# Kernel tuning notes

Measured on AMD Instinct MI355X. Metric: run time of the kernel, lower is better.

The kernel has to match this reference:

```python
import jax, jax.numpy as jnp
import numpy as np

B1, B2, D = 8192, 8192, 128


def _cdist(d1, d2):
    # L2 distance matrix via the |a|^2 + |b|^2 - 2ab expansion (GEMM-dominant).
    d1_sq = jnp.sum(d1 * d1, axis=1, keepdims=True)          # (B1, 1)
    d2_sq = jnp.sum(d2 * d2, axis=1, keepdims=True)          # (B2, 1)
    dm = d1_sq + d2_sq.T - 2.0 * (d1 @ d2.T)                 # (B1, B2)
    return jnp.sqrt(jnp.clip(dm, 0.0))


def setup_inputs() -> dict:
    key = jax.random.key(0)
    k1, k2 = jax.random.split(key)
    desc1 = jax.random.normal(k1, (B1, D), dtype=jnp.float32)
    desc2 = jax.random.normal(k2, (B2, D), dtype=jnp.float32)
    return {"desc1": desc1, "desc2": desc2}


def reference(desc1, desc2):
    # DescriptorMatcher(match_mode='nn'): nearest neighbor in desc2 for each desc1.
    dm = _cdist(desc1, desc2)                                # (B1, B2)
    idxs_in_2 = jnp.argmin(dm, axis=1)                       # (B1,)
    match_dists = jnp.take_along_axis(dm, idxs_in_2[:, None], axis=1)  # (B1, 1)
    idxs_in_1 = jnp.arange(dm.shape[0], dtype=jnp.int64 if jax.config.jax_enable_x64 else jnp.int32)
    matches_idxs = jnp.stack([idxs_in_1, idxs_in_2.astype(idxs_in_1.dtype)], axis=1)  # (B1, 2)
    return match_dists, matches_idxs
```

## Files before the change

kernel.cpp:

```cpp
#include <hip/hip_runtime.h>
#include <cstdint>

#define NB1 8192
#define NB2 8192
#define DDIM 128
#define KROW 256
#define NKITER 12

using half8   = __attribute__((ext_vector_type(8))) _Float16;
using half4   = __attribute__((ext_vector_type(4))) _Float16;
using float4v = __attribute__((ext_vector_type(4))) float;

typedef __attribute__((address_space(3))) void       lds_void;
typedef const __attribute__((address_space(1))) void glb_void;

__device__ inline unsigned long long packkey(float v, int j) {
  unsigned u = __float_as_uint(v);
  u = (u & 0x80000000u) ? ~u : (u | 0x80000000u);
  return ((unsigned long long)u << 32) | (unsigned)j;
}

__device__ __forceinline__ int a_src(int kt) { return (kt < 8) ? kt : kt - 8; }
__device__ __forceinline__ int b_src(int kt) { return (kt < 4) ? kt : kt - 4; }

__global__ __launch_bounds__(256) void convert_kernel(
    const float* __restrict__ d1, const float* __restrict__ d2,
    _Float16* __restrict__ A2, _Float16* __restrict__ B2,
    float* __restrict__ asq, float* __restrict__ bsq,
    unsigned long long* __restrict__ packed) {
  int gid  = blockIdx.x * 256 + threadIdx.x;
  int wv   = gid >> 6;
  int lane = gid & 63;
  int rowc = 2 * wv + (lane >> 5);
  bool isA = rowc < NB1;
  const float* src = isA ? d1 : d2;
  int row = isA ? rowc : rowc - NB1;
  int k4  = (lane & 31) * 4;

  float4 v = *(const float4*)&src[row * DDIM + k4];
  _Float16 h0 = (_Float16)v.x, h1 = (_Float16)v.y;
  _Float16 h2 = (_Float16)v.z, h3 = (_Float16)v.w;
  half4 hh = {h0, h1, h2, h3};
  half4 ll = {(_Float16)(v.x - (float)h0), (_Float16)(v.y - (float)h1),
              (_Float16)(v.z - (float)h2), (_Float16)(v.w - (float)h3)};

  _Float16* dst = (isA ? A2 : B2) + (size_t)row * KROW;
  *(half4*)&dst[k4]       = hh;
  *(half4*)&dst[128 + k4] = ll;

  float s = v.x * v.x + v.y * v.y + v.z * v.z + v.w * v.w;
  #pragma unroll
  for (int off = 16; off > 0; off >>= 1) s += __shfl_xor(s, off, 64);
  if ((lane & 31) == 0) (isA ? asq : bsq)[row] = s;

  if (gid < NB1) packed[gid] = 0xFFFFFFFFFFFFFFFFull;
}

__global__ __launch_bounds__(256, 3) void mfma_match_kernel(
    const _Float16* __restrict__ A2, const _Float16* __restrict__ B2,
    const float* __restrict__ bsq, unsigned long long* __restrict__ packed) {
  __shared__ unsigned long long smem[2 * 128 * 17];
  _Float16* Asb = (_Float16*)smem;
  _Float16* Bsb = (_Float16*)smem + 8192;

  const int t    = threadIdx.x;
  const int lane = t & 63;
  const int wid  = t >> 6;
  const int wm = wid >> 1, wn = wid & 1;
  const int lx = lane & 15, q = lane >> 4;

  const int id = blockIdx.x;
  const int xc = id & 7, kk = id >> 3;
  const int bx = ((kk >> 3) & 7) * 8 + xc;
  const int by = (kk & 7) + ((kk >> 6) & 7) * 8;
  const int row0 = bx * 128, col0 = by * 128;

  const int sA   = wid * 2;
  const int rloc = lane >> 2;
  const int qch  = ((lane & 3) - (rloc >> 1)) & 3;
  const int rA0  = sA * 16 + rloc;
  const int kofs = qch * 8;

  float4v acc[4][4];
  #pragma unroll
  for (int r = 0; r < 4; ++r)
    #pragma unroll
    for (int c = 0; c < 4; ++c) acc[r][c] = (float4v){0.f, 0.f, 0.f, 0.f};

  float bq[4]; int jc[4];
  #pragma unroll
  for (int c = 0; c < 4; ++c) {
    jc[c] = col0 + wn * 64 + 16 * c + lx;
    bq[c] = bsq[jc[c]];
  }

  auto stage = [&](int kt, int buf) {
    const _Float16* ga =
        A2 + (size_t)(row0 + rA0) * KROW + a_src(kt) * 32 + kofs;
    __builtin_amdgcn_global_load_lds((glb_void*)ga,
        (lds_void*)(Asb + buf * 4096 + sA * 512), 16, 0, 0);
    __builtin_amdgcn_global_load_lds((glb_void*)(ga + 16 * KROW),
        (lds_void*)(Asb + buf * 4096 + (sA + 1) * 512), 16, 0, 0);
    const _Float16* gb =
        B2 + (size_t)(col0 + rA0) * KROW + b_src(kt) * 32 + kofs;
    __builtin_amdgcn_global_load_lds((glb_void*)gb,
        (lds_void*)(Bsb + buf * 4096 + sA * 512), 16, 0, 0);
    __builtin_amdgcn_global_load_lds((glb_void*)(gb + 16 * KROW),
        (lds_void*)(Bsb + buf * 4096 + (sA + 1) * 512), 16, 0, 0);
  };

  stage(0, 0);

  const int sw = ((q + (lx >> 1)) & 3) * 8;

  #pragma unroll
  for (int kt = 0; kt < NKITER; ++kt) {
    __syncthreads();
    if (kt < NKITER - 1) stage(kt + 1, (kt + 1) & 1);
    const _Float16* Ab = Asb + (kt & 1) * 4096;
    const _Float16* Bb = Bsb + (kt & 1) * 4096;
    half8 af[4], bf[4];
    #pragma unroll
    for (int r = 0; r < 4; ++r)
      af[r] = *(const half8*)&Ab[(wm * 64 + 16 * r + lx) * 32 + sw];
    #pragma unroll
    for (int c = 0; c < 4; ++c)
      bf[c] = *(const half8*)&Bb[(wn * 64 + 16 * c + lx) * 32 + sw];
    #pragma unroll
    for (int r = 0; r < 4; ++r)
      #pragma unroll
      for (int c = 0; c < 4; ++c)
        acc[r][c] = __builtin_amdgcn_mfma_f32_16x16x32_f16(
            af[r], bf[c], acc[r][c], 0, 0, 0);
  }

  __syncthreads();
  #pragma unroll
  for (int r = 0; r < 4; ++r) {
    #pragma unroll
    for (int reg = 0; reg < 4; ++reg) {
      float bv = 1e30f; int bj = 0;
      #pragma unroll
      for (int c = 0; c < 4; ++c) {
        float val = fmaf(-2.f, acc[r][c][reg], bq[c]);
        if (val < bv) { bv = val; bj = jc[c]; }
      }
      int mrow = wm * 64 + 16 * r + 4 * q + reg;
      smem[(wn * 128 + mrow) * 17 + lx] = packkey(bv, bj);
    }
  }
  __syncthreads();
  if (t < 128) {
    unsigned long long best = ~0ull;
    #pragma unroll
    for (int w = 0; w < 2; ++w)
      #pragma unroll
      for (int x = 0; x < 16; ++x) {
        unsigned long long k = smem[(w * 128 + t) * 17 + x];
        if (k < best) best = k;
      }
    atomicMin(&packed[row0 + t], best);
  }
}

__global__ __launch_bounds__(256) void out_kernel(
    const unsigned long long* __restrict__ packed,
    const float* __restrict__ asq, float* __restrict__ out) {
  int r = blockIdx.x * 256 + threadIdx.x;
  unsigned long long best = packed[r];
  unsigned u = (unsigned)(best >> 32);
  u = (u & 0x80000000u) ? (u & 0x7fffffffu) : ~u;
  float val  = __uint_as_float(u);
  float dist = sqrtf(fmaxf(asq[r] + val, 0.f));
  int j = (int)(unsigned)(best & 0xffffffffu);
  out[r]               = dist;
  out[NB1 + 2 * r]     = (float)r;
  out[NB1 + 2 * r + 1] = (float)j;
}

extern "C" void kernel_launch(void* const* d_in, const int* in_sizes, int n_in,
                              void* d_out, int out_size, void* d_ws, size_t ws_size,
                              hipStream_t stream) {
  const float* d1 = (const float*)d_in[0];
  const float* d2 = (const float*)d_in[1];
  float* out = (float*)d_out;

  char* w = (char*)d_ws;
  float* asq = (float*)w;
  float* bsq = (float*)(w + 32768);
  _Float16* A2 = (_Float16*)(w + 65536);
  _Float16* B2 = (_Float16*)(w + 65536 + 4194304);
  unsigned long long* packed =
      (unsigned long long*)(w + 65536 + 2 * 4194304);

  convert_kernel<<<(NB1 + NB2) / 8, 256, 0, stream>>>(
      d1, d2, A2, B2, asq, bsq, packed);

  mfma_match_kernel<<<(NB1 / 128) * (NB2 / 128), 256, 0, stream>>>(
      A2, B2, bsq, packed);

  out_kernel<<<NB1 / 256, 256, 0, stream>>>(packed, asq, out);
}
```

Before: 123.5 us.

## Double K-tile depth per stage and fuse output finalization via last-block counter

Each main-loop stage now loads a 64-wide K slab instead of 32 and issues two MFMAs per fragment pair, which halves the number of barrier-separated iterations. LDS per block grows to 64KB and occupancy drops from 3 to 2 blocks per CU, with a wider XOR swizzle over 8 chunks. The separate output kernel is removed: a per-row-block atomic counter lets the last finishing column block decode the packed argmin and write distances and indices. This saves one launch but adds a fence and atomics at the end of every block.

```diff
diff --git a/kernel.cpp b/kernel.cpp
--- a/kernel.cpp
+++ b/kernel.cpp
@@ -5,7 +5,7 @@
 #define NB2 8192
 #define DDIM 128
 #define KROW 256
-#define NKITER 12
+#define NKITER 6
 
 using half8   = __attribute__((ext_vector_type(8))) _Float16;
 using half4   = __attribute__((ext_vector_type(4))) _Float16;
@@ -20,14 +20,14 @@
   return ((unsigned long long)u << 32) | (unsigned)j;
 }
 
-__device__ __forceinline__ int a_src(int kt) { return (kt < 8) ? kt : kt - 8; }
-__device__ __forceinline__ int b_src(int kt) { return (kt < 4) ? kt : kt - 4; }
+__device__ __forceinline__ int a_unit(int kt) { return (kt < 4) ? kt : kt - 4; }
+__device__ __forceinline__ int b_unit(int kt) { return (kt < 2) ? kt : kt - 2; }
 
 __global__ __launch_bounds__(256) void convert_kernel(
     const float* __restrict__ d1, const float* __restrict__ d2,
     _Float16* __restrict__ A2, _Float16* __restrict__ B2,
     float* __restrict__ asq, float* __restrict__ bsq,
-    unsigned long long* __restrict__ packed) {
+    unsigned long long* __restrict__ packed, int* __restrict__ cnt) {
   int gid  = blockIdx.x * 256 + threadIdx.x;
   int wv   = gid >> 6;
   int lane = gid & 63;
@@ -54,14 +54,19 @@
   if ((lane & 31) == 0) (isA ? asq : bsq)[row] = s;
 
   if (gid < NB1) packed[gid] = 0xFFFFFFFFFFFFFFFFull;
-}
-
-__global__ __launch_bounds__(256, 3) void mfma_match_kernel(
+  if (gid < NB1 / 128) cnt[gid] = 0;
+}
+
+__global__ __launch_bounds__(256, 2) void mfma_match_kernel(
     const _Float16* __restrict__ A2, const _Float16* __restrict__ B2,
-    const float* __restrict__ bsq, unsigned long long* __restrict__ packed) {
-  __shared__ unsigned long long smem[2 * 128 * 17];
-  _Float16* Asb = (_Float16*)smem;
-  _Float16* Bsb = (_Float16*)smem + 8192;
+    const float* __restrict__ asq, const float* __restrict__ bsq,
+    unsigned long long* __restrict__ packed, int* __restrict__ cnt,
+    float* __restrict__ out) {
+  __shared__ char smem_raw[65536];
+  _Float16* Asb = (_Float16*)smem_raw;
+  _Float16* Bsb = (_Float16*)smem_raw + 16384;
+  unsigned long long* red = (unsigned long long*)smem_raw;
+  int* flagp = (int*)(smem_raw + 40960);
 
   const int t    = threadIdx.x;
   const int lane = t & 63;
@@ -75,11 +80,8 @@
   const int by = (kk & 7) + ((kk >> 6) & 7) * 8;
   const int row0 = bx * 128, col0 = by * 128;
 
-  const int sA   = wid * 2;
-  const int rloc = lane >> 2;
-  const int qch  = ((lane & 3) - (rloc >> 1)) & 3;
-  const int rA0  = sA * 16 + rloc;
-  const int kofs = qch * 8;
+  const int rowoff = lane >> 3;
+  const int qch8   = ((((lane & 7) - (lane >> 3)) & 7)) * 8;
 
   float4v acc[4][4];
   #pragma unroll
@@ -95,43 +97,53 @@
   }
 
   auto stage = [&](int kt, int buf) {
-    const _Float16* ga =
-        A2 + (size_t)(row0 + rA0) * KROW + a_src(kt) * 32 + kofs;
-    __builtin_amdgcn_global_load_lds((glb_void*)ga,
-        (lds_void*)(Asb + buf * 4096 + sA * 512), 16, 0, 0);
-    __builtin_amdgcn_global_load_lds((glb_void*)(ga + 16 * KROW),
-        (lds_void*)(Asb + buf * 4096 + (sA + 1) * 512), 16, 0, 0);
-    const _Float16* gb =
-        B2 + (size_t)(col0 + rA0) * KROW + b_src(kt) * 32 + kofs;
-    __builtin_amdgcn_global_load_lds((glb_void*)gb,
-        (lds_void*)(Bsb + buf * 4096 + sA * 512), 16, 0, 0);
-    __builtin_amdgcn_global_load_lds((glb_void*)(gb + 16 * KROW),
-        (lds_void*)(Bsb + buf * 4096 + (sA + 1) * 512), 16, 0, 0);
+    const int au = a_unit(kt) * 64 + qch8;
+    const int bu = b_unit(kt) * 64 + qch8;
+    #pragma unroll
+    for (int i = 0; i < 4; ++i) {
+      int R = wid * 32 + i * 8;
+      const _Float16* ga = A2 + (size_t)(row0 + R + rowoff) * KROW + au;
+      __builtin_amdgcn_global_load_lds((glb_void*)ga,
+          (lds_void*)(Asb + buf * 8192 + R * 64), 16, 0, 0);
+      const _Float16* gb = B2 + (size_t)(col0 + R + rowoff) * KROW + bu;
+      __builtin_amdgcn_global_load_lds((glb_void*)gb,
+          (lds_void*)(Bsb + buf * 8192 + R * 64), 16, 0, 0);
+    }
   };
 
   stage(0, 0);
 
-  const int sw = ((q + (lx >> 1)) & 3) * 8;
+  const int s0 = ((q + (lx & 7)) & 7) * 8;
+  const int s1 = (((q + 4) + (lx & 7)) & 7) * 8;
 
   #pragma unroll
   for (int kt = 0; kt < NKITER; ++kt) {
     __syncthreads();
     if (kt < NKITER - 1) stage(kt + 1, (kt + 1) & 1);
-    const _Float16* Ab = Asb + (kt & 1) * 4096;
-    const _Float16* Bb = Bsb + (kt & 1) * 4096;
-    half8 af[4], bf[4];
-    #pragma unroll
-    for (int r = 0; r < 4; ++r)
-      af[r] = *(const half8*)&Ab[(wm * 64 + 16 * r + lx) * 32 + sw];
-    #pragma unroll
-    for (int c = 0; c < 4; ++c)
-      bf[c] = *(const half8*)&Bb[(wn * 64 + 16 * c + lx) * 32 + sw];
+    const _Float16* Ab = Asb + (kt & 1) * 8192;
+    const _Float16* Bb = Bsb + (kt & 1) * 8192;
+    half8 af[4][2], bf[4][2];
+    #pragma unroll
+    for (int r = 0; r < 4; ++r) {
+      int rb = (wm * 64 + 16 * r + lx) * 64;
+      af[r][0] = *(const half8*)&Ab[rb + s0];
+      af[r][1] = *(const half8*)&Ab[rb + s1];
+    }
+    #pragma unroll
+    for (int c = 0; c < 4; ++c) {
+      int rb = (wn * 64 + 16 * c + lx) * 64;
+      bf[c][0] = *(const half8*)&Bb[rb + s0];
+      bf[c][1] = *(const half8*)&Bb[rb + s1];
+    }
     #pragma unroll
     for (int r = 0; r < 4; ++r)
       #pragma unroll
-      for (int c = 0; c < 4; ++c)
+      for (int c = 0; c < 4; ++c) {
         acc[r][c] = __builtin_amdgcn_mfma_f32_16x16x32_f16(
-            af[r], bf[c], acc[r][c], 0, 0, 0);
+            af[r][0], bf[c][0], acc[r][c], 0, 0, 0);
+        acc[r][c] = __builtin_amdgcn_mfma_f32_16x16x32_f16(
+            af[r][1], bf[c][1], acc[r][c], 0, 0, 0);
+      }
   }
 
   __syncthreads();
@@ -146,7 +158,7 @@
         if (val < bv) { bv = val; bj = jc[c]; }
       }
       int mrow = wm * 64 + 16 * r + 4 * q + reg;
-      smem[(wn * 128 + mrow) * 17 + lx] = packkey(bv, bj);
+      red[(wn * 128 + mrow) * 17 + lx] = packkey(bv, bj);
     }
   }
   __syncthreads();
@@ -156,26 +168,29 @@
     for (int w = 0; w < 2; ++w)
       #pragma unroll
       for (int x = 0; x < 16; ++x) {
-        unsigned long long k = smem[(w * 128 + t) * 17 + x];
+        unsigned long long k = red[(w * 128 + t) * 17 + x];
         if (k < best) best = k;
       }
     atomicMin(&packed[row0 + t], best);
   }
-}
-
-__global__ __launch_bounds__(256) void out_kernel(
-    const unsigned long long* __restrict__ packed,
-    const float* __restrict__ asq, float* __restrict__ out) {
-  int r = blockIdx.x * 256 + threadIdx.x;
-  unsigned long long best = packed[r];
-  unsigned u = (unsigned)(best >> 32);
-  u = (u & 0x80000000u) ? (u & 0x7fffffffu) : ~u;
-  float val  = __uint_as_float(u);
-  float dist = sqrtf(fmaxf(asq[r] + val, 0.f));
-  int j = (int)(unsigned)(best & 0xffffffffu);
-  out[r]               = dist;
-  out[NB1 + 2 * r]     = (float)r;
-  out[NB1 + 2 * r + 1] = (float)j;
+
+  __syncthreads();
+  if (t == 0) {
+    __threadfence();
+    *flagp = (atomicAdd(&cnt[bx], 1) == NB2 / 128 - 1);
+  }
+  __syncthreads();
+  if (*flagp && t < 128) {
+    int r = row0 + t;
+    unsigned long long best = atomicMin(&packed[r], ~0ull);
+    unsigned u = (unsigned)(best >> 32);
+    u = (u & 0x80000000u) ? (u & 0x7fffffffu) : ~u;
+    float dist = sqrtf(fmaxf(asq[r] + __uint_as_float(u), 0.f));
+    int j = (int)(unsigned)(best & 0xffffffffu);
+    out[r] = dist;
+    float2 mi = {(float)r, (float)j};
+    *(float2*)&out[NB1 + 2 * r] = mi;
+  }
 }
 
 extern "C" void kernel_launch(void* const* d_in, const int* in_sizes, int n_in,
@@ -192,12 +207,11 @@
   _Float16* B2 = (_Float16*)(w + 65536 + 4194304);
   unsigned long long* packed =
       (unsigned long long*)(w + 65536 + 2 * 4194304);
+  int* cnt = (int*)(w + 65536 + 2 * 4194304 + 65536);
 
   convert_kernel<<<(NB1 + NB2) / 8, 256, 0, stream>>>(
-      d1, d2, A2, B2, asq, bsq, packed);
+      d1, d2, A2, B2, asq, bsq, packed, cnt);
 
   mfma_match_kernel<<<(NB1 / 128) * (NB2 / 128), 256, 0, stream>>>(
-      A2, B2, bsq, packed);
-
-  out_kernel<<<NB1 / 256, 256, 0, stream>>>(packed, asq, out);
-}
+      A2, B2, asq, bsq, packed, cnt, out);
+}
```

New measurement: 179.5 us. 1.45x slower.

## Load MFMA operands directly from global into registers, drop LDS staging

Applied to the files above, without the earlier changes.

Replaces the LDS double-buffered staging via global_load_lds and per-iteration barriers with direct per-wave global loads of the fp16 fragments into registers, using a two-stage register ping-pong to overlap loads with MFMAs. This removes the __syncthreads and LDS traffic from the main loop. In exchange, operand tiles are no longer shared between waves, so each wave fetches its own A and B rows from global/L2 with redundancy, and register pressure rises, which may reduce occupancy.

```diff
diff --git a/kernel.cpp b/kernel.cpp
--- a/kernel.cpp
+++ b/kernel.cpp
@@ -10,9 +10,6 @@
 using half8   = __attribute__((ext_vector_type(8))) _Float16;
 using half4   = __attribute__((ext_vector_type(4))) _Float16;
 using float4v = __attribute__((ext_vector_type(4))) float;
-
-typedef __attribute__((address_space(3))) void       lds_void;
-typedef const __attribute__((address_space(1))) void glb_void;
 
 __device__ inline unsigned long long packkey(float v, int j) {
   unsigned u = __float_as_uint(v);
@@ -60,8 +57,6 @@
     const _Float16* __restrict__ A2, const _Float16* __restrict__ B2,
     const float* __restrict__ bsq, unsigned long long* __restrict__ packed) {
   __shared__ unsigned long long smem[2 * 128 * 17];
-  _Float16* Asb = (_Float16*)smem;
-  _Float16* Bsb = (_Float16*)smem + 8192;
 
   const int t    = threadIdx.x;
   const int lane = t & 63;
@@ -75,11 +70,8 @@
   const int by = (kk & 7) + ((kk >> 6) & 7) * 8;
   const int row0 = bx * 128, col0 = by * 128;
 
-  const int sA   = wid * 2;
-  const int rloc = lane >> 2;
-  const int qch  = ((lane & 3) - (rloc >> 1)) & 3;
-  const int rA0  = sA * 16 + rloc;
-  const int kofs = qch * 8;
+  const _Float16* Abase = A2 + (size_t)(row0 + wm * 64 + lx) * KROW + q * 8;
+  const _Float16* Bbase = B2 + (size_t)(col0 + wn * 64 + lx) * KROW + q * 8;
 
   float4v acc[4][4];
   #pragma unroll
@@ -94,47 +86,35 @@
     bq[c] = bsq[jc[c]];
   }
 
-  auto stage = [&](int kt, int buf) {
-    const _Float16* ga =
-        A2 + (size_t)(row0 + rA0) * KROW + a_src(kt) * 32 + kofs;
-    __builtin_amdgcn_global_load_lds((glb_void*)ga,
-        (lds_void*)(Asb + buf * 4096 + sA * 512), 16, 0, 0);
-    __builtin_amdgcn_global_load_lds((glb_void*)(ga + 16 * KROW),
-        (lds_void*)(Asb + buf * 4096 + (sA + 1) * 512), 16, 0, 0);
-    const _Float16* gb =
-        B2 + (size_t)(col0 + rA0) * KROW + b_src(kt) * 32 + kofs;
-    __builtin_amdgcn_global_load_lds((glb_void*)gb,
-        (lds_void*)(Bsb + buf * 4096 + sA * 512), 16, 0, 0);
-    __builtin_amdgcn_global_load_lds((glb_void*)(gb + 16 * KROW),
-        (lds_void*)(Bsb + buf * 4096 + (sA + 1) * 512), 16, 0, 0);
-  };
+  half8 s0a[4], s0b[4], s1a[4], s1b[4];
 
-  stage(0, 0);
-
-  const int sw = ((q + (lx >> 1)) & 3) * 8;
-
-  #pragma unroll
-  for (int kt = 0; kt < NKITER; ++kt) {
-    __syncthreads();
-    if (kt < NKITER - 1) stage(kt + 1, (kt + 1) & 1);
-    const _Float16* Ab = Asb + (kt & 1) * 4096;
-    const _Float16* Bb = Bsb + (kt & 1) * 4096;
-    half8 af[4], bf[4];
+  auto loadS = [&](half8* fa, half8* fb, int kt) {
+    const int ka = a_src(kt) * 32, kb = b_src(kt) * 32;
     #pragma unroll
     for (int r = 0; r < 4; ++r)
-      af[r] = *(const half8*)&Ab[(wm * 64 + 16 * r + lx) * 32 + sw];
+      fa[r] = *(const half8*)(Abase + (size_t)(16 * r) * KROW + ka);
     #pragma unroll
     for (int c = 0; c < 4; ++c)
-      bf[c] = *(const half8*)&Bb[(wn * 64 + 16 * c + lx) * 32 + sw];
+      fb[c] = *(const half8*)(Bbase + (size_t)(16 * c) * KROW + kb);
+  };
+  auto mfmaS = [&](const half8* fa, const half8* fb) {
     #pragma unroll
     for (int r = 0; r < 4; ++r)
       #pragma unroll
       for (int c = 0; c < 4; ++c)
         acc[r][c] = __builtin_amdgcn_mfma_f32_16x16x32_f16(
-            af[r], bf[c], acc[r][c], 0, 0, 0);
+            fa[r], fb[c], acc[r][c], 0, 0, 0);
+  };
+
+  loadS(s0a, s0b, 0);
+  #pragma unroll
+  for (int kt2 = 0; kt2 < NKITER / 2; ++kt2) {
+    loadS(s1a, s1b, 2 * kt2 + 1);
+    mfmaS(s0a, s0b);
+    if (kt2 < NKITER / 2 - 1) loadS(s0a, s0b, 2 * kt2 + 2);
+    mfmaS(s1a, s1b);
   }
 
-  __syncthreads();
   #pragma unroll
   for (int r = 0; r < 4; ++r) {
     #pragma unroll
@@ -170,8 +150,7 @@
   unsigned long long best = packed[r];
   unsigned u = (unsigned)(best >> 32);
   u = (u & 0x80000000u) ? (u & 0x7fffffffu) : ~u;
-  float val  = __uint_as_float(u);
-  float dist = sqrtf(fmaxf(asq[r] + val, 0.f));
+  float dist = sqrtf(fmaxf(asq[r] + __uint_as_float(u), 0.f));
   int j = (int)(unsigned)(best & 0xffffffffu);
   out[r]               = dist;
   out[NB1 + 2 * r]     = (float)r;
```

After: 258.4 us. 109% more time.
